# Kernel tuning notes

Measured on AMD Instinct MI355X. Metric: run time of the kernel, lower is better.

## Reference

```python
import jax, jax.numpy as jnp
import numpy as np

HIDDEN = 2048
N_EXPERTS = 256
TOP_K = 8
N_GROUP = 8
TOPK_GROUP = 4
GROUP_SIZE = N_EXPERTS // N_GROUP  # 32
AUX_ALPHA = 0.001
Z_ALPHA = 0.0001
TOKENS = 16384


def setup_inputs() -> dict:
    key = jax.random.key(0)
    k1, k2 = jax.random.split(key)
    hidden_states = jax.random.normal(k1, (TOKENS, HIDDEN), dtype=jnp.float32)
    # nn.Linear(hidden, n_experts, bias=False) weight: [n_experts, hidden]
    gate_w = jax.random.normal(k2, (N_EXPERTS, HIDDEN), dtype=jnp.float32) * 0.02
    return {"hidden_states": hidden_states, "gate_w": gate_w}


def reference(hidden_states, gate_w):
    T = hidden_states.shape[0]
    # gate GEMM: [T, E]
    logits = jnp.einsum('th,eh->te', hidden_states, gate_w)
    # grouped top-k: per-group top-(topk_group)
    group_logits = logits.reshape(T, N_GROUP, GROUP_SIZE)
    g_vals, g_idx = jax.lax.top_k(group_logits, TOPK_GROUP)  # [T, G, tg]
    cand_vals = g_vals.reshape(T, N_GROUP * TOPK_GROUP)
    cand_idx = g_idx.reshape(T, N_GROUP * TOPK_GROUP)
    # global top-k over candidates
    topk_logits, pos = jax.lax.top_k(cand_vals, TOP_K)  # [T, K]
    selected_group = pos // TOPK_GROUP
    expert_in_group = jnp.take_along_axis(cand_idx, pos, axis=1)
    topk_idx = selected_group * GROUP_SIZE + expert_in_group  # [T, K]
    topk_weight = jax.nn.softmax(topk_logits, axis=-1)
    # training-mode losses (module defaults: both alphas > 0, train mode)
    probs = jax.nn.softmax(logits, axis=-1)  # [T, E]
    expert_counts = jnp.zeros((N_EXPERTS,), jnp.float32).at[topk_idx.reshape(-1)].add(1.0)
    expert_probs = probs.mean(axis=0)
    aux_loss = jnp.sum(expert_counts / T * expert_probs) * AUX_ALPHA
    z_loss = jnp.mean(jnp.log(probs.sum(axis=0)) ** 2) * Z_ALPHA
    total_aux_loss = aux_loss + z_loss
    return topk_idx, topk_weight, total_aux_loss
```

## Files before the change

kernel.cpp:

```cpp
#include <hip/hip_runtime.h>
#include <math.h>

#define HIDDEN  2048
#define NEXP    256
#define TOPK    8
#define NGROUP  8
#define TKG     4
#define GSZ     32
#define TM      32
#define KC      32
#define NCHUNK  (HIDDEN / KC)
#define LGSTR   (NEXP + 2)

__global__ __launch_bounds__(256, 2) void moe_gate_main(
    const float* __restrict__ X,
    const float* __restrict__ W,
    float* __restrict__ out,
    double* __restrict__ S_ws,
    int* __restrict__ cnt_ws,
    int T)
{
#pragma clang fp contract(off)
    __shared__ __align__(16) float xs[TM][KC];
    __shared__ __align__(16) float pool[TM * LGSTR];
    __shared__ float dmax[TM];
    __shared__ float den[TM];

    const int tid = threadIdx.x;
    const int tg  = tid >> 6;
    const int exq = tid & 63;
    const int t0  = blockIdx.x * TM;
    const int swz = exq & 7;

    float4 acc[8][4];
#pragma unroll
    for (int i = 0; i < 8; ++i)
#pragma unroll
        for (int j = 0; j < 4; ++j) acc[i][j] = make_float4(0.f, 0.f, 0.f, 0.f);

    for (int c = 0; c < NCHUNK; ++c) {
        const int k0 = c * KC;
        __syncthreads();
        {
            const int trow = tid >> 3, col4 = tid & 7;
            const float4 v = *(const float4*)(X + (size_t)(t0 + trow) * HIDDEN + k0 + 4 * col4);
            *(float4*)&xs[trow][4 * col4] = v;
        }
#pragma unroll
        for (int it = 0; it < 8; ++it) {
            const int f4  = it * 256 + tid;
            const int row = f4 >> 3, col4 = f4 & 7;
            const float4 v = *(const float4*)(W + (size_t)row * HIDDEN + k0 + 4 * col4);
            *(float4*)&pool[row * KC + ((col4 ^ (row & 7)) * 4)] = v;
        }
        __syncthreads();
#pragma unroll
        for (int blk = 0; blk < 2; ++blk) {
#pragma unroll
            for (int vv = 3; vv >= 0; --vv) {
                const int k4 = blk * 4 + vv;
                const int sc = (k4 ^ swz) * 4;
                float4 wv[4];
#pragma unroll
                for (int j = 0; j < 4; ++j)
                    wv[j] = *(const float4*)&pool[(exq + 64 * j) * KC + sc];
#pragma unroll
                for (int i = 0; i < 8; ++i) {
                    const float4 xv = *(const float4*)&xs[tg * 8 + i][4 * k4];
#pragma unroll
                    for (int j = 0; j < 4; ++j) {
                        acc[i][j].x = __fadd_rn(acc[i][j].x, __fmul_rn(xv.x, wv[j].x));
                        acc[i][j].y = __fadd_rn(acc[i][j].y, __fmul_rn(xv.y, wv[j].y));
                        acc[i][j].z = __fadd_rn(acc[i][j].z, __fmul_rn(xv.z, wv[j].z));
                        acc[i][j].w = __fadd_rn(acc[i][j].w, __fmul_rn(xv.w, wv[j].w));
                    }
                }
            }
        }
    }

    __syncthreads();
#pragma unroll
    for (int i = 0; i < 8; ++i)
#pragma unroll
        for (int j = 0; j < 4; ++j) {
            const float4 a = acc[i][j];
            pool[(tg * 8 + i) * LGSTR + exq + 64 * j] =
                __fadd_rn(__fadd_rn(a.x, a.y), __fadd_rn(a.z, a.w));
        }
    __syncthreads();

    if (tid < TM) {
        const int t = tid;
        float cv[NGROUP * TKG];
        int   ci[NGROUP * TKG];
        float gmax = -3.0e38f;

        for (int g = 0; g < NGROUP; ++g) {
            float v4[TKG] = { -3.0e38f, -3.0e38f, -3.0e38f, -3.0e38f };
            int   i4[TKG] = { 0, 0, 0, 0 };
            for (int jj = 0; jj < GSZ; ++jj) {
                const float v = pool[t * LGSTR + g * GSZ + jj];
                if (v > gmax) gmax = v;
                if (v > v4[TKG - 1]) {
                    int q = TKG - 1;
                    while (q > 0 && v > v4[q - 1]) {
                        v4[q] = v4[q - 1]; i4[q] = i4[q - 1]; --q;
                    }
                    v4[q] = v; i4[q] = jj;
                }
            }
#pragma unroll
            for (int r = 0; r < TKG; ++r) { cv[g * TKG + r] = v4[r]; ci[g * TKG + r] = i4[r]; }
        }

        float v8[TOPK]; int p8[TOPK];
#pragma unroll
        for (int k = 0; k < TOPK; ++k) { v8[k] = -3.0e38f; p8[k] = 0; }
        for (int p = 0; p < NGROUP * TKG; ++p) {
            const float v = cv[p];
            if (v > v8[TOPK - 1]) {
                int q = TOPK - 1;
                while (q > 0 && v > v8[q - 1]) {
                    v8[q] = v8[q - 1]; p8[q] = p8[q - 1]; --q;
                }
                v8[q] = v; p8[q] = p;
            }
        }

        float w8[TOPK]; float ssum = 0.f;
#pragma unroll
        for (int k = 0; k < TOPK; ++k) {
            w8[k] = expf(v8[k] - v8[0]);
            ssum += w8[k];
        }

        const size_t row = (size_t)(t0 + t) * TOPK;
#pragma unroll
        for (int k = 0; k < TOPK; ++k) {
            const int pos = p8[k];
            const int ex  = (pos >> 2) * GSZ + ci[pos];
            out[row + k] = (float)ex;
            out[(size_t)T * TOPK + row + k] = w8[k] / ssum;
            atomicAdd(&cnt_ws[ex], 1);
        }

        float dsum = 0.f;
        for (int e2 = 0; e2 < NEXP; ++e2)
            dsum += expf(pool[t * LGSTR + e2] - gmax);
        dmax[t] = gmax;
        den[t]  = dsum;
    }
    __syncthreads();

    double part = 0.0;
#pragma unroll
    for (int t = 0; t < TM; ++t)
        part += (double)(expf(pool[t * LGSTR + tid] - dmax[t]) / den[t]);
    atomicAdd(&S_ws[tid], part);
}

__global__ __launch_bounds__(256) void moe_gate_loss(
    const double* __restrict__ S_ws, const int* __restrict__ cnt_ws,
    float* __restrict__ out, int T)
{
    __shared__ double red[NEXP];
    const int e = threadIdx.x;
    const double S = S_ws[e];
    const double c = (double)cnt_ws[e];
    const double Td = (double)T;
    const double aux = (c / Td) * (S / Td);
    double z = log(S); z *= z;

    red[e] = aux; __syncthreads();
    for (int s = 128; s > 0; s >>= 1) { if (e < s) red[e] += red[e + s]; __syncthreads(); }
    const double auxsum = red[0];
    __syncthreads();
    red[e] = z; __syncthreads();
    for (int s = 128; s > 0; s >>= 1) { if (e < s) red[e] += red[e + s]; __syncthreads(); }
    if (e == 0)
        out[(size_t)T * TOPK * 2] = (float)(auxsum * 1.0e-3 + (red[0] / (double)NEXP) * 1.0e-4);
}

extern "C" void kernel_launch(void* const* d_in, const int* in_sizes, int n_in,
                              void* d_out, int out_size, void* d_ws, size_t ws_size,
                              hipStream_t stream)
{
    const float* X = (const float*)d_in[0];
    const float* W = (const float*)d_in[1];
    float* out = (float*)d_out;
    const int T = in_sizes[0] / HIDDEN;

    double* S_ws   = (double*)d_ws;
    int*    cnt_ws = (int*)((char*)d_ws + NEXP * sizeof(double));

    hipMemsetAsync(d_ws, 0, NEXP * (sizeof(double) + sizeof(int)), stream);

    moe_gate_main<<<dim3(T / TM), dim3(256), 0, stream>>>(X, W, out, S_ws, cnt_ws, T);
    moe_gate_loss<<<dim3(1), dim3(256), 0, stream>>>(S_ws, cnt_ws, out, T);
}
```

Measured before the change: 493.1 us.

## Double-buffer gate GEMM tiles with async global-to-LDS loads

Replaces the register-staged loads of the X and W chunks with `__builtin_amdgcn_global_load_lds` direct copies into two LDS buffers. The next chunk is prefetched while the current one is computed, and one barrier per iteration is dropped. The XOR swizzle on W moves to the source address, so each lane writes contiguous LDS. This raises LDS use to about 73 KB per block, and correctness relies on the compiler waiting on the async copies before the next barrier.

```diff
diff --git a/kernel.cpp b/kernel.cpp
--- a/kernel.cpp
+++ b/kernel.cpp
@@ -11,6 +11,14 @@
 #define KC      32
 #define NCHUNK  (HIDDEN / KC)
 #define LGSTR   (NEXP + 2)
+#define WSZ     (NEXP * KC)
+#define XSZ     (TM * KC)
+
+__device__ __forceinline__ void async16(const float* g, float* lds_base) {
+    __builtin_amdgcn_global_load_lds(
+        (const __attribute__((address_space(1))) void*)g,
+        (__attribute__((address_space(3))) void*)lds_base, 16, 0, 0);
+}
 
 __global__ __launch_bounds__(256, 2) void moe_gate_main(
     const float* __restrict__ X,
@@ -21,8 +29,7 @@
     int T)
 {
 #pragma clang fp contract(off)
-    __shared__ __align__(16) float xs[TM][KC];
-    __shared__ __align__(16) float pool[TM * LGSTR];
+    __shared__ __align__(16) float smem[2 * WSZ + 2 * XSZ];
     __shared__ float dmax[TM];
     __shared__ float den[TM];
 
@@ -32,28 +39,38 @@
     const int t0  = blockIdx.x * TM;
     const int swz = exq & 7;
 
+    const int l  = tid & 63;
+    const int lr = l >> 3;
+    const int lc = l & 7;
+    const float* Wsrc = W + (size_t)(tg * 8 + lr) * HIDDEN + 4 * (lc ^ lr);
+    const float* Xsrc = X + (size_t)(t0 + tg * 8 + lr) * HIDDEN + 4 * lc;
+    float* Wdst0 = smem + (tg * 8) * KC;
+    float* Xdst0 = smem + 2 * WSZ + tg * 256;
+
+#define STAGE(c, buf)                                                         \
+    do {                                                                      \
+        const int k0_ = (c) * KC;                                             \
+        _Pragma("unroll")                                                     \
+        for (int it = 0; it < 8; ++it)                                        \
+            async16(Wsrc + (size_t)it * 32 * HIDDEN + k0_,                    \
+                    Wdst0 + (buf) * WSZ + it * 32 * KC);                      \
+        async16(Xsrc + k0_, Xdst0 + (buf) * XSZ);                             \
+    } while (0)
+
     float4 acc[8][4];
 #pragma unroll
     for (int i = 0; i < 8; ++i)
 #pragma unroll
         for (int j = 0; j < 4; ++j) acc[i][j] = make_float4(0.f, 0.f, 0.f, 0.f);
 
+    STAGE(0, 0);
+
     for (int c = 0; c < NCHUNK; ++c) {
-        const int k0 = c * KC;
+        const int cur = c & 1;
         __syncthreads();
-        {
-            const int trow = tid >> 3, col4 = tid & 7;
-            const float4 v = *(const float4*)(X + (size_t)(t0 + trow) * HIDDEN + k0 + 4 * col4);
-            *(float4*)&xs[trow][4 * col4] = v;
-        }
-#pragma unroll
-        for (int it = 0; it < 8; ++it) {
-            const int f4  = it * 256 + tid;
-            const int row = f4 >> 3, col4 = f4 & 7;
-            const float4 v = *(const float4*)(W + (size_t)row * HIDDEN + k0 + 4 * col4);
-            *(float4*)&pool[row * KC + ((col4 ^ (row & 7)) * 4)] = v;
-        }
-        __syncthreads();
+        if (c + 1 < NCHUNK) STAGE(c + 1, cur ^ 1);
+        const float* ws_ = smem + cur * WSZ;
+        const float* xs_ = smem + 2 * WSZ + cur * XSZ;
 #pragma unroll
         for (int blk = 0; blk < 2; ++blk) {
 #pragma unroll
@@ -63,10 +80,10 @@
                 float4 wv[4];
 #pragma unroll
                 for (int j = 0; j < 4; ++j)
-                    wv[j] = *(const float4*)&pool[(exq + 64 * j) * KC + sc];
+                    wv[j] = *(const float4*)(ws_ + (exq + 64 * j) * KC + sc);
 #pragma unroll
                 for (int i = 0; i < 8; ++i) {
-                    const float4 xv = *(const float4*)&xs[tg * 8 + i][4 * k4];
+                    const float4 xv = *(const float4*)(xs_ + (tg * 8 + i) * KC + 4 * k4);
 #pragma unroll
                     for (int j = 0; j < 4; ++j) {
                         acc[i][j].x = __fadd_rn(acc[i][j].x, __fmul_rn(xv.x, wv[j].x));
@@ -78,8 +95,10 @@
             }
         }
     }
-
-    __syncthreads();
+#undef STAGE
+
+    __syncthreads();
+    float* pool = smem;
 #pragma unroll
     for (int i = 0; i < 8; ++i)
 #pragma unroll
```

After: 601.0 us. 21.9% more time.
